# Performance work log

Measured on AMD Instinct MI355X. Metric: run time of the kernel, lower is better.

Reference implementation:

```python
import jax, jax.numpy as jnp
import numpy as np

B, DX, DY, H, K = 16384, 128, 128, 2048, 16
MIN_BIN = 1e-3   # min bin width/height (nflows convention)
MIN_DERIV = 1e-3  # min knot derivative


def setup_inputs() -> dict:
    key = jax.random.key(0)
    k0, k1, k2, k3 = jax.random.split(key, 4)
    x = jax.random.normal(k0, (B, DX), jnp.float32)
    y = jax.random.uniform(k1, (B, DY), jnp.float32, minval=1e-4, maxval=1.0 - 1e-4)
    W1 = jax.random.normal(k2, (DX, H), jnp.float32) / np.sqrt(DX).astype(np.float32)
    b1 = jnp.zeros((H,), jnp.float32)
    W2 = jax.random.normal(k3, (H, DY * (3 * K + 1)), jnp.float32) / np.sqrt(H).astype(np.float32)
    b2 = jnp.zeros((DY * (3 * K + 1),), jnp.float32)
    return {"x": x, "y": y, "W1": W1, "b1": b1, "W2": W2, "b2": b2}


def _rq_spline(y, pdf):
    # y: [B, D] in (0,1); pdf: [B, D, 3K+1] unnormalized spline params
    w_un, h_un, d_un = pdf[..., :K], pdf[..., K:2 * K], pdf[..., 2 * K:]
    widths = MIN_BIN + (1.0 - K * MIN_BIN) * jax.nn.softmax(w_un, axis=-1)   # [B,D,K]
    heights = MIN_BIN + (1.0 - K * MIN_BIN) * jax.nn.softmax(h_un, axis=-1)  # [B,D,K]
    derivs = MIN_DERIV + jax.nn.softplus(d_un)                               # [B,D,K+1]

    pad = [(0, 0), (0, 0), (1, 0)]
    cw = jnp.pad(jnp.cumsum(widths, axis=-1), pad)    # knot x-positions [B,D,K+1]
    ch = jnp.pad(jnp.cumsum(heights, axis=-1), pad)   # knot y-positions [B,D,K+1]

    # data-dependent bin lookup (searchsorted equivalent, vectorized)
    idx = jnp.clip(jnp.sum(y[..., None] >= cw, axis=-1) - 1, 0, K - 1)  # [B,D]
    g = lambda a: jnp.take_along_axis(a, idx[..., None], axis=-1)[..., 0]
    xk, yk = g(cw), g(ch)
    wk, hk = g(widths), g(heights)
    dk = g(derivs)
    dk1 = jnp.take_along_axis(derivs, idx[..., None] + 1, axis=-1)[..., 0]

    s = hk / wk                      # bin slope
    t = (y - xk) / wk                # theta in [0,1]
    omt = 1.0 - t
    denom = s + (dk1 + dk - 2.0 * s) * t * omt
    out = yk + hk * (s * t * t + dk * t * omt) / denom
    deriv = s * s * (dk1 * t * t + 2.0 * s * t * omt + dk * omt * omt) / (denom * denom)
    dlogp = jnp.sum(jnp.log(deriv), axis=-1, keepdims=True)  # [B,1]
    return out, dlogp


def reference(x, y, W1, b1, W2, b2):
    # conditioner MLP: x -> spline params
    h = jax.nn.relu(x @ W1 + b1)
    pdf = (h @ W2 + b2).reshape(x.shape[0], DY, 3 * K + 1)
    return _rq_spline(y, pdf)
```

## Files before the change

### kernel.cpp

```cpp
#include <hip/hip_runtime.h>
#include <hip/hip_fp16.h>
#include <cstdint>
#include <cstddef>

#define B_ROWS 16384
#define DX 128
#define DYDIM 128
#define HDIM 2048
#define NPARAM 49
#define NCOL 6272
#define NTILES 26
#define W2PROWS (NTILES * 256)

typedef __attribute__((ext_vector_type(8))) _Float16 half8v;
typedef __attribute__((ext_vector_type(4))) float f32x4;

__global__ void k_f32_to_f16(const float* __restrict__ in, _Float16* __restrict__ out, int n) {
  int i = blockIdx.x * 256 + threadIdx.x;
  if (i < n) out[i] = (_Float16)in[i];
}

__global__ void k_transpose_f16(const float* __restrict__ in, _Float16* __restrict__ out, int R, int C) {
  __shared__ float tile[32][33];
  int c0 = blockIdx.x * 32, r0 = blockIdx.y * 32;
  int tx = threadIdx.x;
  for (int i = threadIdx.y; i < 32; i += 8)
    tile[i][tx] = in[(size_t)(r0 + i) * C + c0 + tx];
  __syncthreads();
  for (int i = threadIdx.y; i < 32; i += 8)
    out[(size_t)(c0 + i) * R + r0 + tx] = (_Float16)tile[tx][i];
}

__global__ void k_transpose_perm(const float* __restrict__ in, _Float16* __restrict__ out) {
  __shared__ float tile[32][33];
  int c0 = blockIdx.x * 32, r0 = blockIdx.y * 32;
  int tx = threadIdx.x;
  for (int i = threadIdx.y; i < 32; i += 8)
    tile[i][tx] = in[(size_t)(r0 + i) * NCOL + c0 + tx];
  __syncthreads();
  for (int i = threadIdx.y; i < 32; i += 8) {
    int g = c0 + i;
    int t = g / 245;
    int cc = g - t * 245;
    out[(size_t)(t * 256 + cc) * HDIM + r0 + tx] = (_Float16)tile[tx][i];
  }
}

__global__ __launch_bounds__(256) void k_gemm1(
    const _Float16* __restrict__ A, const _Float16* __restrict__ Bt,
    const float* __restrict__ bias, _Float16* __restrict__ C,
    int M, int N, int K) {
  __shared__ _Float16 Abuf[128 * 32];
  __shared__ _Float16 Bbuf[128 * 32];
  const int t = threadIdx.x;
  const int l = t & 63;
  const int w = t >> 6;
  int bx = blockIdx.x, by = blockIdx.y;
  {
    const int nx = gridDim.x;
    const int nwg = nx * gridDim.y;
    const int lin = by * nx + bx;
    const int cpx = nwg >> 3;
    const int sw = (lin & 7) * cpx + (lin >> 3);
    bx = sw % nx;
    by = sw / nx;
  }
  const int tileM = by * 128;
  const int tileN = bx * 128;
  const int wm = w >> 1, wn = w & 1;
  const int srow = w * 16 + (l >> 2);
  const int skel = (l & 3) * 8;
  const char* Ag = (const char*)(A + (size_t)(tileM + srow) * K + skel);
  const char* Bg = (const char*)(Bt + (size_t)(tileN + srow) * K + skel);
  const size_t gRowStep = (size_t)64 * K * 2;
  auto ldsA = (__attribute__((address_space(3))) char*)Abuf;
  auto ldsB = (__attribute__((address_space(3))) char*)Bbuf;
  const int ldsBase = w * 1024;
  f32x4 acc[4][4];
#pragma unroll
  for (int i = 0; i < 4; ++i)
#pragma unroll
    for (int j = 0; j < 4; ++j) acc[i][j] = (f32x4){0.f, 0.f, 0.f, 0.f};
  const int nk = K >> 5;
#define STAGE1(kt)                                                                             \
  do {                                                                                         \
    size_t koff = (size_t)(kt) * 64;                                                           \
    __builtin_amdgcn_global_load_lds(                                                          \
        (const __attribute__((address_space(1))) uint32_t*)(Ag + koff),                        \
        (__attribute__((address_space(3))) uint32_t*)(ldsA + ldsBase), 16, 0, 0);              \
    __builtin_amdgcn_global_load_lds(                                                          \
        (const __attribute__((address_space(1))) uint32_t*)(Ag + koff + gRowStep),             \
        (__attribute__((address_space(3))) uint32_t*)(ldsA + 4096 + ldsBase), 16, 0, 0);       \
    __builtin_amdgcn_global_load_lds(                                                          \
        (const __attribute__((address_space(1))) uint32_t*)(Bg + koff),                        \
        (__attribute__((address_space(3))) uint32_t*)(ldsB + ldsBase), 16, 0, 0);              \
    __builtin_amdgcn_global_load_lds(                                                          \
        (const __attribute__((address_space(1))) uint32_t*)(Bg + koff + gRowStep),             \
        (__attribute__((address_space(3))) uint32_t*)(ldsB + 4096 + ldsBase), 16, 0, 0);       \
  } while (0)
  STAGE1(0);
  const int abase = (wm * 64 + (l & 15)) * 32 + (l >> 4) * 8;
  const int bbase = (wn * 64 + (l & 15)) * 32 + (l >> 4) * 8;
  for (int kt = 0; kt < nk; ++kt) {
    __syncthreads();
    half8v av[4], bv[4];
#pragma unroll
    for (int mf = 0; mf < 4; ++mf)
      av[mf] = *(const half8v*)((const _Float16*)Abuf + abase + mf * 512);
#pragma unroll
    for (int nf = 0; nf < 4; ++nf)
      bv[nf] = *(const half8v*)((const _Float16*)Bbuf + bbase + nf * 512);
#pragma unroll
    for (int mf = 0; mf < 4; ++mf)
#pragma unroll
      for (int nf = 0; nf < 4; ++nf)
        acc[mf][nf] = __builtin_amdgcn_mfma_f32_16x16x32_f16(av[mf], bv[nf], acc[mf][nf], 0, 0, 0);
    __syncthreads();
    if (kt + 1 < nk) STAGE1(kt + 1);
  }
#undef STAGE1
  const int crow0 = tileM + wm * 64 + (l >> 4) * 4;
  const int ccol0 = tileN + wn * 64 + (l & 15);
#pragma unroll
  for (int nf = 0; nf < 4; ++nf) {
    const int col = ccol0 + nf * 16;
    const float bvv = bias[col];
#pragma unroll
    for (int mf = 0; mf < 4; ++mf) {
#pragma unroll
      for (int j = 0; j < 4; ++j) {
        const int row = crow0 + mf * 16 + j;
        float v = fmaxf(acc[mf][nf][j] + bvv, 0.f);
        C[(size_t)row * N + col] = (_Float16)v;
      }
    }
  }
}

__global__ __launch_bounds__(512, 2) void k_gemm2s(
    const _Float16* __restrict__ A, const _Float16* __restrict__ Bt,
    const float* __restrict__ bias, const float* __restrict__ y,
    float* __restrict__ outp, float* __restrict__ gpart, int M) {
  constexpr int K = HDIM;
  constexpr int K2 = K * 2;
  constexpr int NT = K / 64;
  constexpr int ITERS = NT / 2;

  __shared__ char smem[131072];
  __shared__ float red[512];

  const int t = threadIdx.x;
  const int l = t & 63;
  const int w = t >> 6;
  const int wm = w >> 2;
  const int wn = w & 3;
  const int rlo = l & 15;
  const int khi = l >> 4;
  const int wOff = w * 1024;

  int bx = blockIdx.x, by = blockIdx.y;
  {
    const int lin = by * 26 + bx;
    const int xcd = lin & 7;
    const int slot = lin >> 3;
    bx = slot >> 3;
    by = xcd * 8 + (slot & 7);
  }
  const int tileM = by * 256;
  const int tileN = bx * 256;

  int rowj[2], kbj[2];
#pragma unroll
  for (int j = 0; j < 2; ++j) {
    const int phys = j * 8192 + t * 16;
    const int b = phys ^ (((phys >> 9) & 1) << 5);
    rowj[j] = ((b >> 11) << 4) + ((b >> 6) & 15);
    kbj[j] = (((b >> 10) & 1) << 6) + (b & 63);
  }
  const char* pA[2][2];
  const char* pB[2][2];
#pragma unroll
  for (int half = 0; half < 2; ++half)
#pragma unroll
    for (int j = 0; j < 2; ++j) {
      pA[half][j] = (const char*)A + (size_t)(tileM + half * 128 + rowj[j]) * K2 + kbj[j];
      pB[half][j] = (const char*)Bt + (size_t)(tileN + half * 128 + rowj[j]) * K2 + kbj[j];
    }

  auto lds3 = (__attribute__((address_space(3))) char*)smem;

#define LDSA(d, half) ((d) * 32768 + (half) * 16384)
#define LDSB(d, half) (65536 + (d) * 32768 + (half) * 16384)
#define GLDS(srcp, ldsoff)                                                                   \
  __builtin_amdgcn_global_load_lds(                                                           \
      (const __attribute__((address_space(1))) uint32_t*)(srcp),                              \
      (__attribute__((address_space(3))) uint32_t*)(lds3 + (ldsoff) + wOff), 16, 0, 0)
#define STG(op, d, half, kt)                                                                  \
  do {                                                                                        \
    GLDS(p##op[half][0] + (size_t)(kt) * 128, LDS##op(d, half));                              \
    GLDS(p##op[half][1] + (size_t)(kt) * 128, LDS##op(d, half) + 8192);                       \
  } while (0)
#define VM(n) asm volatile("s_waitcnt vmcnt(" #n ")" ::: "memory")
#define NOSTG ((void)0)
#define NOW ((void)0)
#define CFENCE asm volatile("" ::: "memory")

  const int swz = (rlo & 8) ? 32 : 0;
  const int lane16 = rlo * 64 + ((khi * 16) ^ swz);
  const int aW = wm * 8192 + lane16;
  const int bW = 65536 + wn * 4096 + lane16;

  half8v b000, b001, b010, b011, b100, b101, b110, b111;
  f32x4 acc[8][4];
#pragma unroll
  for (int i = 0; i < 8; ++i)
#pragma unroll
    for (int j = 0; j < 4; ++j) acc[i][j] = (f32x4){0.f, 0.f, 0.f, 0.f};

#define MF(fi, gj, av, bv) \
  acc[fi][gj] = __builtin_amdgcn_mfma_f32_16x16x32_f16(av, bv, acc[fi][gj], 0, 0, 0)

#define PHX(d, q, LOADB, WAITS, ...)                                                          \
  do {                                                                                        \
    const int aB = (d) * 32768 + ((q) >> 1) * 16384 + ((q) & 1) * 4096 + aW;                  \
    half8v a00 = *(const half8v*)(smem + aB);                                                 \
    half8v a01 = *(const half8v*)(smem + aB + 1024);                                          \
    half8v a10 = *(const half8v*)(smem + aB + 2048);                                          \
    half8v a11 = *(const half8v*)(smem + aB + 3072);                                          \
    if (LOADB) {                                                                              \
      const int bB = (d) * 32768 + bW;                                                        \
      b000 = *(const half8v*)(smem + bB);                                                     \
      b001 = *(const half8v*)(smem + bB + 1024);                                              \
      b010 = *(const half8v*)(smem + bB + 2048);                                              \
      b011 = *(const half8v*)(smem + bB + 3072);                                              \
      b100 = *(const half8v*)(smem + bB + 16384);                                             \
      b101 = *(const half8v*)(smem + bB + 17408);                                             \
      b110 = *(const half8v*)(smem + bB + 18432);                                             \
      b111 = *(const half8v*)(smem + bB + 19456);                                             \
    }                                                                                         \
    __VA_ARGS__;                                                                              \
    WAITS;                                                                                    \
    CFENCE;                                                                                   \
    __builtin_amdgcn_s_barrier();                                                             \
    CFENCE;                                                                                   \
    __builtin_amdgcn_s_setprio(1);                                                            \
    {                                                                                         \
      constexpr int f0 = ((q) >> 1) * 4 + ((q) & 1) * 2;                                      \
      MF(f0 + 0, 0, a00, b000); MF(f0 + 0, 1, a00, b010);                                     \
      MF(f0 + 0, 2, a00, b100); MF(f0 + 0, 3, a00, b110);                                     \
      MF(f0 + 1, 0, a10, b000); MF(f0 + 1, 1, a10, b010);                                     \
      MF(f0 + 1, 2, a10, b100); MF(f0 + 1, 3, a10, b110);                                     \
      MF(f0 + 0, 0, a01, b001); MF(f0 + 0, 1, a01, b011);                                     \
      MF(f0 + 0, 2, a01, b101); MF(f0 + 0, 3, a01, b111);                                     \
      MF(f0 + 1, 0, a11, b001); MF(f0 + 1, 1, a11, b011);                                     \
      MF(f0 + 1, 2, a11, b101); MF(f0 + 1, 3, a11, b111);                                     \
    }                                                                                         \
    __builtin_amdgcn_s_setprio(0);                                                            \
    CFENCE;                                                                                   \
    __builtin_amdgcn_s_barrier();                                                             \
  } while (0)

  STG(B, 0, 0, 0);
  STG(B, 0, 1, 0);
  STG(A, 0, 0, 0);
  STG(A, 0, 1, 0);
  STG(B, 1, 0, 1);
  STG(B, 1, 1, 1);
  STG(A, 1, 0, 1);
  VM(6);
  CFENCE;
  __builtin_amdgcn_s_barrier();

  for (int it = 0; it < ITERS - 1; ++it) {
    const int kt = 2 * it;
    PHX(0, 0, 1, NOW, STG(A, 1, 1, kt + 1));
    PHX(0, 1, 0, NOW, STG(B, 0, 0, kt + 2));
    PHX(0, 2, 0, NOW, STG(B, 0, 1, kt + 2); STG(A, 0, 0, kt + 2));
    PHX(0, 3, 0, VM(8), NOSTG);
    PHX(1, 0, 1, NOW, STG(A, 0, 1, kt + 2));
    PHX(1, 1, 0, VM(10), STG(B, 1, 0, kt + 3));
    PHX(1, 2, 0, NOW, STG(B, 1, 1, kt + 3); STG(A, 1, 0, kt + 3));
    PHX(1, 3, 0, VM(6), NOSTG);
  }
  PHX(0, 0, 1, NOW, STG(A, 1, 1, NT - 1));
  PHX(0, 1, 0, NOW, NOSTG);
  PHX(0, 2, 0, NOW, NOSTG);
  PHX(0, 3, 0, VM(2), NOSTG);
  PHX(1, 0, 1, NOW, NOSTG);
  PHX(1, 1, 0, VM(0), NOSTG);
  PHX(1, 2, 0, NOW, NOSTG);
  PHX(1, 3, 0, NOW, NOSTG);

#undef PHX
#undef MF
#undef STG
#undef GLDS
#undef LDSA
#undef LDSB

  const int RCt = (bx < 25) ? 245 : 147;
  const int nd  = (bx < 25) ? 5 : 3;

#pragma unroll
  for (int fi = 0; fi < 8; ++fi) {
    const int r0l = (((fi >> 2) * 2 + wm) << 6) + ((fi & 3) << 4) + khi * 4;
#pragma unroll
    for (int gj = 0; gj < 4; ++gj) {
      const int c = (((gj >> 1) * 4 + wn) << 5) + ((gj & 1) << 4) + rlo;
      if (c < RCt) {
        const float bvv = bias[245 * bx + c];
        const int cb = c * 512;
        const int cs = (c & 31) << 4;
#pragma unroll
        for (int jp = 0; jp < 2; ++jp) {
          const int r = r0l + jp * 2;
          const unsigned short lo =
              __builtin_bit_cast(unsigned short, (_Float16)(acc[fi][gj][jp * 2] + bvv));
          const unsigned short hi =
              __builtin_bit_cast(unsigned short, (_Float16)(acc[fi][gj][jp * 2 + 1] + bvv));
          *(uint32_t*)(smem + cb + ((2 * r) ^ cs)) = (uint32_t)lo | ((uint32_t)hi << 16);
        }
      }
    }
  }
  __syncthreads();

  const int r = t & 255;
  const int rg = tileM + r;
  float yv_[3];
#pragma unroll
  for (int pass = 0; pass < 3; ++pass) {
    const int d = pass * 2 + (t >> 8);
    yv_[pass] = (d < nd) ? y[(size_t)rg * DYDIM + 5 * bx + d] : 0.f;
  }

#define LDC(p) ((float)*(const _Float16*)(smem + (size_t)(dD * 49 + (p)) * 512 + \
                                          ((2 * r) ^ (((dD * 49 + (p)) & 31) << 4))))
  float lsum = 0.f;
#pragma unroll
  for (int pass = 0; pass < 3; ++pass) {
    const int dD = pass * 2 + (t >> 8);
    if (dD < nd) {
      float qw[16], qh[16], qd[17];
#pragma unroll
      for (int p = 0; p < 16; ++p) { qw[p] = LDC(p); qh[p] = LDC(16 + p); }
#pragma unroll
      for (int p = 0; p < 17; ++p) qd[p] = LDC(32 + p);

      float mw = qw[0], mh = qh[0];
#pragma unroll
      for (int p = 1; p < 16; ++p) { mw = fmaxf(mw, qw[p]); mh = fmaxf(mh, qh[p]); }
      float ew[16], eh[16];
      float sw2 = 0.f, sh = 0.f;
#pragma unroll
      for (int p = 0; p < 16; ++p) {
        ew[p] = __expf(qw[p] - mw);
        eh[p] = __expf(qh[p] - mh);
        sw2 += ew[p];
        sh += eh[p];
      }
      const float rw = 0.984f / sw2, rh = 0.984f / sh;
      const float yv = yv_[pass];

      float cws = 0.f, chs = 0.f, xk = 0.f, yk = 0.f, wk = 1.f, hk = 1.f;
      float du0 = qd[0], du1 = qd[1];
#pragma unroll
      for (int j = 0; j < 16; ++j) {
        float wj = 0.001f + rw * ew[j];
        float hj = 0.001f + rh * eh[j];
        if (yv >= cws) { xk = cws; yk = chs; wk = wj; hk = hj; du0 = qd[j]; du1 = qd[j + 1]; }
        cws += wj;
        chs += hj;
      }
      const float dk  = 0.001f + fmaxf(du0, 0.f) + log1pf(__expf(-fabsf(du0)));
      const float dk1 = 0.001f + fmaxf(du1, 0.f) + log1pf(__expf(-fabsf(du1)));

      const float s = hk / wk;
      const float tt = (yv - xk) / wk;
      const float omt = 1.f - tt;
      const float dnm = s + (dk1 + dk - 2.f * s) * tt * omt;
      const float o = yk + hk * (s * tt * tt + dk * tt * omt) / dnm;
      const float dr = s * s * (dk1 * tt * tt + 2.f * s * tt * omt + dk * omt * omt) / (dnm * dnm);

      outp[(size_t)rg * DYDIM + 5 * bx + dD] = o;
      lsum += __logf(dr);
    }
  }
#undef LDC
  red[t] = lsum;
  __syncthreads();
  if (t < 256)
    gpart[(size_t)bx * B_ROWS + (tileM + t)] = red[t] + red[t + 256];
}

__global__ void k_dlogp_reduce(const float* __restrict__ gpart, float* __restrict__ dlogp) {
  int b = blockIdx.x * 256 + threadIdx.x;
  float s = 0.f;
  for (int tt = 0; tt < NTILES; ++tt) s += gpart[(size_t)tt * B_ROWS + b];
  dlogp[b] = s;
}

extern "C" void kernel_launch(void* const* d_in, const int* in_sizes, int n_in,
                              void* d_out, int out_size, void* d_ws, size_t ws_size,
                              hipStream_t stream) {
  const float* x  = (const float*)d_in[0];
  const float* y  = (const float*)d_in[1];
  const float* W1 = (const float*)d_in[2];
  const float* b1 = (const float*)d_in[3];
  const float* W2 = (const float*)d_in[4];
  const float* b2 = (const float*)d_in[5];
  float* out = (float*)d_out;
  float* dlogp = out + (size_t)B_ROWS * DYDIM;

  char* ws = (char*)d_ws;
  _Float16* w2p = (_Float16*)ws;
  _Float16* h   = w2p + (size_t)W2PROWS * HDIM;
  _Float16* xb  = h + (size_t)B_ROWS * HDIM;
  _Float16* w1t = xb + (size_t)B_ROWS * DX;
  float* gpart  = (float*)(w1t + (size_t)HDIM * DX);

  k_f32_to_f16<<<(B_ROWS * DX + 255) / 256, 256, 0, stream>>>(x, xb, B_ROWS * DX);
  k_transpose_f16<<<dim3(HDIM / 32, DX / 32), dim3(32, 8), 0, stream>>>(W1, w1t, DX, HDIM);
  k_transpose_perm<<<dim3(NCOL / 32, HDIM / 32), dim3(32, 8), 0, stream>>>(W2, w2p);

  k_gemm1<<<dim3(HDIM / 128, B_ROWS / 128), 256, 0, stream>>>(
      xb, w1t, b1, h, B_ROWS, HDIM, DX);

  k_gemm2s<<<dim3(NTILES, B_ROWS / 256), 512, 0, stream>>>(
      h, w2p, b2, y, out, gpart, B_ROWS);

  k_dlogp_reduce<<<B_ROWS / 256, 256, 0, stream>>>(gpart, dlogp);
}
```

Measured before the change: 489.9 us.

## Double-buffer A-fragment LDS reads one phase ahead of MFMAs

The A-operand LDS reads for the next phase are now issued after each barrier, alternating between two register sets, so they overlap with the current phase's MFMAs instead of sitting before the barrier on the critical path. B fragments are still read at the start of each K-half. This adds eight live half8 registers, which may raise register pressure. Correctness depends on the reads landing after the data is ready and before the next stage writes over it.

```diff
diff --git a/kernel.cpp b/kernel.cpp
--- a/kernel.cpp
+++ b/kernel.cpp
@@ -203,6 +203,7 @@
 #define VM(n) asm volatile("s_waitcnt vmcnt(" #n ")" ::: "memory")
 #define NOSTG ((void)0)
 #define NOW ((void)0)
+#define NORD ((void)0)
 #define CFENCE asm volatile("" ::: "memory")
 
   const int swz = (rlo & 8) ? 32 : 0;
@@ -211,6 +212,9 @@
   const int bW = 65536 + wn * 4096 + lane16;
 
   half8v b000, b001, b010, b011, b100, b101, b110, b111;
+  half8v s0_0, s0_1, s0_2, s0_3;
+  half8v s1_0, s1_1, s1_2, s1_3;
+
   f32x4 acc[8][4];
 #pragma unroll
   for (int i = 0; i < 8; ++i)
@@ -220,41 +224,51 @@
 #define MF(fi, gj, av, bv) \
   acc[fi][gj] = __builtin_amdgcn_mfma_f32_16x16x32_f16(av, bv, acc[fi][gj], 0, 0, 0)
 
-#define PHX(d, q, LOADB, WAITS, ...)                                                          \
+#define RDA(S, d, q)                                                                          \
   do {                                                                                        \
     const int aB = (d) * 32768 + ((q) >> 1) * 16384 + ((q) & 1) * 4096 + aW;                  \
-    half8v a00 = *(const half8v*)(smem + aB);                                                 \
-    half8v a01 = *(const half8v*)(smem + aB + 1024);                                          \
-    half8v a10 = *(const half8v*)(smem + aB + 2048);                                          \
-    half8v a11 = *(const half8v*)(smem + aB + 3072);                                          \
-    if (LOADB) {                                                                              \
-      const int bB = (d) * 32768 + bW;                                                        \
-      b000 = *(const half8v*)(smem + bB);                                                     \
-      b001 = *(const half8v*)(smem + bB + 1024);                                              \
-      b010 = *(const half8v*)(smem + bB + 2048);                                              \
-      b011 = *(const half8v*)(smem + bB + 3072);                                              \
-      b100 = *(const half8v*)(smem + bB + 16384);                                             \
-      b101 = *(const half8v*)(smem + bB + 17408);                                             \
-      b110 = *(const half8v*)(smem + bB + 18432);                                             \
-      b111 = *(const half8v*)(smem + bB + 19456);                                             \
-    }                                                                                         \
-    __VA_ARGS__;                                                                              \
+    S##_0 = *(const half8v*)(smem + aB);                                                      \
+    S##_1 = *(const half8v*)(smem + aB + 1024);                                               \
+    S##_2 = *(const half8v*)(smem + aB + 2048);                                               \
+    S##_3 = *(const half8v*)(smem + aB + 3072);                                               \
+  } while (0)
+
+#define HDRB(d)                                                                               \
+  do {                                                                                        \
+    const int bB = (d) * 32768 + bW;                                                          \
+    b000 = *(const half8v*)(smem + bB);                                                       \
+    b001 = *(const half8v*)(smem + bB + 1024);                                                \
+    b010 = *(const half8v*)(smem + bB + 2048);                                                \
+    b011 = *(const half8v*)(smem + bB + 3072);                                                \
+    b100 = *(const half8v*)(smem + bB + 16384);                                               \
+    b101 = *(const half8v*)(smem + bB + 17408);                                               \
+    b110 = *(const half8v*)(smem + bB + 18432);                                               \
+    b111 = *(const half8v*)(smem + bB + 19456);                                               \
+  } while (0)
+
+#define MFQ(q, S)                                                                             \
+  {                                                                                           \
+    constexpr int f0 = ((q) >> 1) * 4 + ((q) & 1) * 2;                                        \
+    MF(f0 + 0, 0, S##_0, b000); MF(f0 + 0, 1, S##_0, b010);                                   \
+    MF(f0 + 0, 2, S##_0, b100); MF(f0 + 0, 3, S##_0, b110);                                   \
+    MF(f0 + 1, 0, S##_2, b000); MF(f0 + 1, 1, S##_2, b010);                                   \
+    MF(f0 + 1, 2, S##_2, b100); MF(f0 + 1, 3, S##_2, b110);                                   \
+    MF(f0 + 0, 0, S##_1, b001); MF(f0 + 0, 1, S##_1, b011);                                   \
+    MF(f0 + 0, 2, S##_1, b101); MF(f0 + 0, 3, S##_1, b111);                                   \
+    MF(f0 + 1, 0, S##_3, b001); MF(f0 + 1, 1, S##_3, b011);                                   \
+    MF(f0 + 1, 2, S##_3, b101); MF(f0 + 1, 3, S##_3, b111);                                   \
+  }
+
+#define PH2(STAGES, WAITS, RD, MFMAS)                                                         \
+  do {                                                                                        \
+    STAGES;                                                                                   \
     WAITS;                                                                                    \
     CFENCE;                                                                                   \
     __builtin_amdgcn_s_barrier();                                                             \
     CFENCE;                                                                                   \
+    RD;                                                                                       \
     __builtin_amdgcn_s_setprio(1);                                                            \
-    {                                                                                         \
-      constexpr int f0 = ((q) >> 1) * 4 + ((q) & 1) * 2;                                      \
-      MF(f0 + 0, 0, a00, b000); MF(f0 + 0, 1, a00, b010);                                     \
-      MF(f0 + 0, 2, a00, b100); MF(f0 + 0, 3, a00, b110);                                     \
-      MF(f0 + 1, 0, a10, b000); MF(f0 + 1, 1, a10, b010);                                     \
-      MF(f0 + 1, 2, a10, b100); MF(f0 + 1, 3, a10, b110);                                     \
-      MF(f0 + 0, 0, a01, b001); MF(f0 + 0, 1, a01, b011);                                     \
-      MF(f0 + 0, 2, a01, b101); MF(f0 + 0, 3, a01, b111);                                     \
-      MF(f0 + 1, 0, a11, b001); MF(f0 + 1, 1, a11, b011);                                     \
-      MF(f0 + 1, 2, a11, b101); MF(f0 + 1, 3, a11, b111);                                     \
-    }                                                                                         \
+    MFMAS;                                                                                    \
     __builtin_amdgcn_s_setprio(0);                                                            \
     CFENCE;                                                                                   \
     __builtin_amdgcn_s_barrier();                                                             \
@@ -270,28 +284,32 @@
   VM(6);
   CFENCE;
   __builtin_amdgcn_s_barrier();
+  RDA(s0, 0, 0);
 
   for (int it = 0; it < ITERS - 1; ++it) {
     const int kt = 2 * it;
-    PHX(0, 0, 1, NOW, STG(A, 1, 1, kt + 1));
-    PHX(0, 1, 0, NOW, STG(B, 0, 0, kt + 2));
-    PHX(0, 2, 0, NOW, STG(B, 0, 1, kt + 2); STG(A, 0, 0, kt + 2));
-    PHX(0, 3, 0, VM(8), NOSTG);
-    PHX(1, 0, 1, NOW, STG(A, 0, 1, kt + 2));
-    PHX(1, 1, 0, VM(10), STG(B, 1, 0, kt + 3));
-    PHX(1, 2, 0, NOW, STG(B, 1, 1, kt + 3); STG(A, 1, 0, kt + 3));
-    PHX(1, 3, 0, VM(6), NOSTG);
-  }
-  PHX(0, 0, 1, NOW, STG(A, 1, 1, NT - 1));
-  PHX(0, 1, 0, NOW, NOSTG);
-  PHX(0, 2, 0, NOW, NOSTG);
-  PHX(0, 3, 0, VM(2), NOSTG);
-  PHX(1, 0, 1, NOW, NOSTG);
-  PHX(1, 1, 0, VM(0), NOSTG);
-  PHX(1, 2, 0, NOW, NOSTG);
-  PHX(1, 3, 0, NOW, NOSTG);
-
-#undef PHX
+    PH2(HDRB(0); STG(A, 1, 1, kt + 1), NOW, RDA(s1, 0, 1), MFQ(0, s0));
+    PH2(STG(B, 0, 0, kt + 2), NOW, RDA(s0, 0, 2), MFQ(1, s1));
+    PH2(STG(B, 0, 1, kt + 2); STG(A, 0, 0, kt + 2), NOW, RDA(s1, 0, 3), MFQ(2, s0));
+    PH2(NOSTG, VM(8), RDA(s0, 1, 0), MFQ(3, s1));
+    PH2(HDRB(1); STG(A, 0, 1, kt + 2), NOW, RDA(s1, 1, 1), MFQ(0, s0));
+    PH2(STG(B, 1, 0, kt + 3), VM(10), RDA(s0, 1, 2), MFQ(1, s1));
+    PH2(STG(B, 1, 1, kt + 3); STG(A, 1, 0, kt + 3), NOW, RDA(s1, 1, 3), MFQ(2, s0));
+    PH2(NOSTG, VM(6), RDA(s0, 0, 0), MFQ(3, s1));
+  }
+  PH2(HDRB(0); STG(A, 1, 1, NT - 1), NOW, RDA(s1, 0, 1), MFQ(0, s0));
+  PH2(NOSTG, NOW, RDA(s0, 0, 2), MFQ(1, s1));
+  PH2(NOSTG, NOW, RDA(s1, 0, 3), MFQ(2, s0));
+  PH2(NOSTG, VM(2), RDA(s0, 1, 0), MFQ(3, s1));
+  PH2(HDRB(1), NOW, RDA(s1, 1, 1), MFQ(0, s0));
+  PH2(NOSTG, VM(0), RDA(s0, 1, 2), MFQ(1, s1));
+  PH2(NOSTG, NOW, RDA(s1, 1, 3), MFQ(2, s0));
+  PH2(NOSTG, NOW, NORD, MFQ(3, s1));
+
+#undef PH2
+#undef MFQ
+#undef HDRB
+#undef RDA
 #undef MF
 #undef STG
 #undef GLDS
```

New measurement: 547.4 us. +11.8%, slower.
